# Optimization experiments

Hardware: AMD Instinct MI355X
Metric: run time of the kernel (lower is better)

The kernel has to match this reference:

```python
import jax, jax.numpy as jnp
import numpy as np
import math

B, S, E, H, D, L, HF = 8, 1024, 512, 8, 64, 6, 2048
EPS = 1e-5
INF = 1000000.0


def _gelu(x):
    # custom tanh-approx gelu from the source
    return 0.5 * x * (1 + jnp.tanh(math.sqrt(2 / math.pi) * (x + 0.044715 * x ** 3)))


def _layernorm(x, gamma, beta):
    mean = jnp.mean(x, axis=-1, keepdims=True)
    var = jnp.mean((x - mean) ** 2, axis=-1, keepdims=True)
    return gamma * ((x - mean) / jnp.sqrt(var + EPS)) + beta


def setup_inputs() -> dict:
    key = jax.random.key(0)
    ks = jax.random.split(key, 10)
    scale = 0.02
    x = jax.random.normal(ks[0], (B, S, E), dtype=jnp.float32)
    att_mask = jax.random.randint(ks[1], (B, S), 0, 2) == 1
    WQ = jax.random.normal(ks[2], (L, E, E), dtype=jnp.float32) * scale
    WK = jax.random.normal(ks[3], (L, E, E), dtype=jnp.float32) * scale
    WV = jax.random.normal(ks[4], (L, E, E), dtype=jnp.float32) * scale
    WO = jax.random.normal(ks[5], (L, E, E), dtype=jnp.float32) * scale
    W1 = jax.random.normal(ks[6], (L, HF, E), dtype=jnp.float32) * scale
    W2 = jax.random.normal(ks[7], (L, E, HF), dtype=jnp.float32) * scale
    bQ = jnp.zeros((L, E)); bK = jnp.zeros((L, E)); bV = jnp.zeros((L, E)); bO = jnp.zeros((L, E))
    b1 = jnp.zeros((L, HF)); b2 = jnp.zeros((L, E))
    g1 = jnp.ones((L, E)); bt1 = jnp.zeros((L, E))
    g2 = jnp.ones((L, E)); bt2 = jnp.zeros((L, E))
    return {"x": x, "att_mask": att_mask, "WQ": WQ, "bQ": bQ, "WK": WK, "bK": bK,
            "WV": WV, "bV": bV, "WO": WO, "bO": bO, "W1": W1, "b1": b1, "W2": W2,
            "b2": b2, "g1": g1, "bt1": bt1, "g2": g2, "bt2": bt2}


def reference(x, att_mask, WQ, bQ, WK, bK, WV, bV, WO, bO, W1, b1, W2, b2, g1, bt1, g2, bt2):
    # additive mask applied to scores: score - (~mask) * infinity, broadcast over (B,1,1,S)
    inv_att = (~att_mask).astype(x.dtype)[:, None, None, :] * INF
    inv_sqrt_d = 1.0 / math.sqrt(D)
    for l in range(L):
        # --- multi-head self-attention ---
        q = (jnp.einsum('bse,fe->bsf', x, WQ[l]) + bQ[l]).reshape(B, S, H, D).transpose(0, 2, 1, 3)
        k = (jnp.einsum('bse,fe->bsf', x, WK[l]) + bK[l]).reshape(B, S, H, D).transpose(0, 2, 1, 3)
        v = (jnp.einsum('bse,fe->bsf', x, WV[l]) + bV[l]).reshape(B, S, H, D).transpose(0, 2, 1, 3)
        score = jnp.einsum('bhsd,bhtd->bhst', q, k) * inv_sqrt_d - inv_att
        attn = jax.nn.softmax(score, axis=-1)
        o = jnp.einsum('bhst,bhtd->bhsd', attn, v).transpose(0, 2, 1, 3).reshape(B, S, E)
        o = jnp.einsum('bse,fe->bsf', o, WO[l]) + bO[l]
        x = _layernorm(x + o, g1[l], bt1[l])
        # --- pointwise feed-forward ---
        h = _gelu(jnp.einsum('bse,fe->bsf', x, W1[l]) + b1[l])
        f = jnp.einsum('bsf,ef->bse', h, W2[l]) + b2[l]
        x = _layernorm(x + f, g2[l], bt2[l])
    return x
```

## Files before the change

### kernel.cpp

```cpp
#include <hip/hip_runtime.h>
#include <cstdint>
#include <cstddef>

#define NB 8
#define NS 1024
#define NE 512
#define NH 8
#define ND 64
#define NL 6
#define NHF 2048
#define NROW (NB*NS)

typedef __bf16 bf16_t;
typedef __bf16 bf8v __attribute__((ext_vector_type(8)));
typedef __bf16 bf4v __attribute__((ext_vector_type(4)));
typedef float  f4   __attribute__((ext_vector_type(4)));

extern "C" __device__ float __ocml_native_exp2_f32(float);
#define EXP2F __ocml_native_exp2_f32
#define LOG2E 1.4426950408889634f

__device__ __forceinline__ void async_copy16(const bf16_t* g, bf16_t* l) {
    __builtin_amdgcn_global_load_lds(
        (const __attribute__((address_space(1))) void*)g,
        (__attribute__((address_space(3))) void*)l,
        16, 0, 0);
}

__device__ __forceinline__ float gelu_f(float x) {
    const float s = fmaf(0.044715f * x * x, x, x);
    const float e = EXP2F(-2.3022081995f * s);
    return x * __builtin_amdgcn_rcpf(1.0f + e);
}

template<int BN, int ACT, int OUT>
__device__ __forceinline__ void gemm_core(
    bf16_t* __restrict__ sm,
    const bf16_t* __restrict__ A, const bf16_t* __restrict__ Bm,
    const float* __restrict__ bias, bf16_t* __restrict__ Cb,
    int m0, int n0, int N, int K)
{
    constexpr int JN = BN / 32, WSPAN = BN / 2;
    bf16_t* As = sm;
    bf16_t* Bs = sm + 2*128*64;
    const int tid  = threadIdx.x;
    const int lane = tid & 63;
    const int wave = tid >> 6;
    const int wm = wave >> 1, wn = wave & 1;
    const int quad = lane >> 4, l16 = lane & 15;
    const int srow = tid >> 3;
    const int scol = (((tid & 7) ^ (srow & 7)) << 3);

    f4 acc[4][JN] = {};

    const bf16_t* Ag = A  + (size_t)(m0 + srow) * K + scol;
    const bf16_t* Bg = Bm + (size_t)(n0 + srow) * K + scol;
    const int sw = (l16 & 7);

    auto stage = [&](int buf, int kt) {
#pragma unroll
        for (int r = 0; r < 4; ++r)
            async_copy16(Ag + (size_t)r * 32 * K + kt, As + buf*8192 + tid*8 + r*2048);
#pragma unroll
        for (int r = 0; r < BN/32; ++r)
            async_copy16(Bg + (size_t)r * 32 * K + kt, Bs + buf*(BN*64) + tid*8 + r*2048);
    };

    stage(0, 0);
    int buf = 0;
    for (int kt = 0; kt < K; kt += 64, buf ^= 1) {
        __syncthreads();
        if (kt + 64 < K) stage(buf ^ 1, kt + 64);
        const bf16_t* Ab = As + buf*8192;
        const bf16_t* Bb = Bs + buf*(BN*64);
#pragma unroll
        for (int s = 0; s < 2; ++s) {
            const int c8 = ((s*4 + quad) ^ sw) * 8;
            bf8v af[4], bfv[JN];
#pragma unroll
            for (int i = 0; i < 4; ++i)
                af[i] = *(const bf8v*)(Ab + (wm*64 + i*16 + l16)*64 + c8);
#pragma unroll
            for (int j = 0; j < JN; ++j)
                bfv[j] = *(const bf8v*)(Bb + (wn*WSPAN + j*16 + l16)*64 + c8);
#pragma unroll
            for (int i = 0; i < 4; ++i)
#pragma unroll
                for (int j = 0; j < JN; ++j)
                    acc[i][j] = __builtin_amdgcn_mfma_f32_16x16x32_bf16(bfv[j], af[i], acc[i][j], 0, 0, 0);
        }
    }

#pragma unroll
    for (int i = 0; i < 4; ++i) {
        const int mi = m0 + wm*64 + i*16 + l16;
        const size_t m = (size_t)mi;
#pragma unroll
        for (int j = 0; j < JN; ++j) {
            const int nb = n0 + wn*WSPAN + j*16 + quad*4;
            const f4 bv = *(const f4*)(bias + nb);
            f4 v = acc[i][j] + bv;
            if (ACT) {
#pragma unroll
                for (int r = 0; r < 4; ++r) v[r] = gelu_f(v[r]);
            }
            bf4v* cp = (bf4v*)(Cb + m * (size_t)N + nb);
            bf4v o;
            if (OUT == 2) {
                const bf4v old = *cp;
#pragma unroll
                for (int r = 0; r < 4; ++r) o[r] = (bf16_t)((float)old[r] + v[r]);
            } else {
#pragma unroll
                for (int r = 0; r < 4; ++r) o[r] = (bf16_t)v[r];
            }
            *cp = o;
        }
    }
}

template<int BN, int ACT, int OUT>
__global__ __launch_bounds__(256)
void gemm_bt_k(const bf16_t* __restrict__ A, const bf16_t* __restrict__ Bm,
               const float* __restrict__ bias, bf16_t* __restrict__ Cb, int N, int K)
{
    __shared__ __align__(16) bf16_t smem[2*128*64 + 2*BN*64];
    gemm_core<BN, ACT, OUT>(smem, A, Bm, bias, Cb,
                            blockIdx.x * 128, blockIdx.y * BN, N, K);
}

__global__ __launch_bounds__(512, 2)
void gemm_rmw_ln_k(const bf16_t* __restrict__ A, const bf16_t* __restrict__ Bm,
                   const float* __restrict__ bias, bf16_t* __restrict__ xb,
                   const float* __restrict__ gamma, const float* __restrict__ beta,
                   float* __restrict__ fout, int wf, int K)
{
    __shared__ __align__(16) bf16_t As[2*32*64];
    __shared__ __align__(16) bf16_t Bs[2*512*64];
    __shared__ float wsum[8][32], wssq[8][32];
    const int tid  = threadIdx.x;
    const int lane = tid & 63;
    const int wave = tid >> 6;
    const int quad = lane >> 4, l16 = lane & 15;
    const int sw = l16 & 7;
    const int srow = tid >> 3;
    const int scol = ((tid & 7) ^ (srow & 7)) << 3;
    const int m0 = blockIdx.x * 32;

    const bf16_t* Ag = A  + (size_t)(m0 + srow) * K + scol;
    const bf16_t* Bg = Bm + (size_t)srow * K + scol;

    f4 acc[2][4] = {};

    auto stage = [&](int buf, int kt) {
        if (tid < 256)
            async_copy16(Ag + kt, As + buf*2048 + tid*8);
#pragma unroll
        for (int r = 0; r < 8; ++r)
            async_copy16(Bg + (size_t)r * 64 * K + kt, Bs + buf*32768 + (r*512 + tid)*8);
    };

    stage(0, 0);
    int buf = 0;
    for (int kt = 0; kt < K; kt += 64, buf ^= 1) {
        __syncthreads();
        if (kt + 64 < K) stage(buf ^ 1, kt + 64);
        const bf16_t* Ab = As + buf*2048;
        const bf16_t* Bb = Bs + buf*32768;
#pragma unroll
        for (int s = 0; s < 2; ++s) {
            const int c8 = ((s*4 + quad) ^ sw) * 8;
            bf8v af[2], bfv[4];
#pragma unroll
            for (int i = 0; i < 2; ++i)
                af[i] = *(const bf8v*)(Ab + (i*16 + l16)*64 + c8);
#pragma unroll
            for (int j = 0; j < 4; ++j)
                bfv[j] = *(const bf8v*)(Bb + (wave*64 + j*16 + l16)*64 + c8);
#pragma unroll
            for (int i = 0; i < 2; ++i)
#pragma unroll
                for (int j = 0; j < 4; ++j)
                    acc[i][j] = __builtin_amdgcn_mfma_f32_16x16x32_bf16(bfv[j], af[i], acc[i][j], 0, 0, 0);
        }
    }

    f4 v[2][4];
    float ps[2], pss[2];
#pragma unroll
    for (int i = 0; i < 2; ++i) {
        ps[i] = 0.f; pss[i] = 0.f;
        const size_t m = (size_t)(m0 + i*16 + l16);
#pragma unroll
        for (int j = 0; j < 4; ++j) {
            const int nb = wave*64 + j*16 + quad*4;
            const f4 bv = *(const f4*)(bias + nb);
            const bf4v old = *(const bf4v*)(xb + m * NE + nb);
            f4 t = acc[i][j] + bv;
#pragma unroll
            for (int r = 0; r < 4; ++r) {
                t[r] += (float)old[r];
                ps[i]  += t[r];
                pss[i] += t[r] * t[r];
            }
            v[i][j] = t;
        }
        ps[i]  += __shfl_xor(ps[i], 16, 64);
        ps[i]  += __shfl_xor(ps[i], 32, 64);
        pss[i] += __shfl_xor(pss[i], 16, 64);
        pss[i] += __shfl_xor(pss[i], 32, 64);
    }
    if (quad == 0) {
#pragma unroll
        for (int i = 0; i < 2; ++i) {
            wsum[wave][i*16 + l16] = ps[i];
            wssq[wave][i*16 + l16] = pss[i];
        }
    }
    __syncthreads();
#pragma unroll
    for (int i = 0; i < 2; ++i) {
        const int row = i*16 + l16;
        float s = 0.f, ss = 0.f;
#pragma unroll
        for (int w = 0; w < 8; ++w) { s += wsum[w][row]; ss += wssq[w][row]; }
        const float mean = s * (1.0f / NE);
        const float var  = ss * (1.0f / NE) - mean * mean;
        const float inv  = rsqrtf(var + 1e-5f);
        const size_t m = (size_t)(m0 + row);
#pragma unroll
        for (int j = 0; j < 4; ++j) {
            const int nb = wave*64 + j*16 + quad*4;
            const f4 gm = *(const f4*)(gamma + nb);
            const f4 bt = *(const f4*)(beta + nb);
            f4 o;
            bf4v ob;
#pragma unroll
            for (int r = 0; r < 4; ++r) {
                o[r]  = gm[r] * ((v[i][j][r] - mean) * inv) + bt[r];
                ob[r] = (bf16_t)o[r];
            }
            *(bf4v*)(xb + m * NE + nb) = ob;
            if (wf) *(f4*)(fout + m * NE + nb) = o;
        }
    }
}

__global__ __launch_bounds__(256, 2)
void gemm_qkv_k(const bf16_t* __restrict__ A,
                const bf16_t* __restrict__ wq, const bf16_t* __restrict__ wk, const bf16_t* __restrict__ wv,
                const float* __restrict__ bq, const float* __restrict__ bk, const float* __restrict__ bv,
                bf16_t* __restrict__ Q, bf16_t* __restrict__ K, bf16_t* __restrict__ Vt,
                const unsigned short* __restrict__ rank)
{
    __shared__ __align__(16) bf16_t As_[2*128*64];
    __shared__ __align__(16) bf16_t Bs_[3][2*64*64];
    const int tid  = threadIdx.x;
    const int lane = tid & 63;
    const int wave = tid >> 6;
    const int wm = wave >> 1, wn = wave & 1;
    const int quad = lane >> 4, l16 = lane & 15;
    const int sw = l16 & 7;
    const int srow = tid >> 3;
    const int scol = (((tid & 7) ^ (srow & 7)) << 3);
    const int m0 = blockIdx.x * 128, n0 = blockIdx.y * 64;

    const bf16_t* Ag = A + (size_t)(m0 + srow) * NE + scol;
    const bf16_t* Wg0 = wq + (size_t)(n0 + srow) * NE + scol;
    const bf16_t* Wg1 = wk + (size_t)(n0 + srow) * NE + scol;
    const bf16_t* Wg2 = wv + (size_t)(n0 + srow) * NE + scol;

    f4 acc[3][4][2] = {};

    auto stage = [&](int buf, int kt) {
#pragma unroll
        for (int r = 0; r < 4; ++r)
            async_copy16(Ag + (size_t)r*32*NE + kt, As_ + buf*8192 + tid*8 + r*2048);
#pragma unroll
        for (int r = 0; r < 2; ++r) {
            async_copy16(Wg0 + (size_t)r*32*NE + kt, Bs_[0] + buf*4096 + tid*8 + r*2048);
            async_copy16(Wg1 + (size_t)r*32*NE + kt, Bs_[1] + buf*4096 + tid*8 + r*2048);
            async_copy16(Wg2 + (size_t)r*32*NE + kt, Bs_[2] + buf*4096 + tid*8 + r*2048);
        }
    };

    stage(0, 0);
    int buf = 0;
    for (int kt = 0; kt < NE; kt += 64, buf ^= 1) {
        __syncthreads();
        if (kt + 64 < NE) stage(buf ^ 1, kt + 64);
        const bf16_t* Ab = As_ + buf*8192;
#pragma unroll
        for (int s = 0; s < 2; ++s) {
            const int c8 = ((s*4 + quad) ^ sw) * 8;
            bf8v af[4];
#pragma unroll
            for (int i = 0; i < 4; ++i)
                af[i] = *(const bf8v*)(Ab + (wm*64 + i*16 + l16)*64 + c8);
#pragma unroll
            for (int mat = 0; mat < 3; ++mat) {
                const bf16_t* Bb = Bs_[mat] + buf*4096;
                const bf8v b0 = *(const bf8v*)(Bb + (wn*32      + l16)*64 + c8);
                const bf8v b1 = *(const bf8v*)(Bb + (wn*32 + 16 + l16)*64 + c8);
                if (mat < 2) {
#pragma unroll
                    for (int i = 0; i < 4; ++i) {
                        acc[mat][i][0] = __builtin_amdgcn_mfma_f32_16x16x32_bf16(b0, af[i], acc[mat][i][0], 0, 0, 0);
                        acc[mat][i][1] = __builtin_amdgcn_mfma_f32_16x16x32_bf16(b1, af[i], acc[mat][i][1], 0, 0, 0);
                    }
                } else {
#pragma unroll
                    for (int i = 0; i < 4; ++i) {
                        acc[2][i][0] = __builtin_amdgcn_mfma_f32_16x16x32_bf16(af[i], b0, acc[2][i][0], 0, 0, 0);
                        acc[2][i][1] = __builtin_amdgcn_mfma_f32_16x16x32_bf16(af[i], b1, acc[2][i][1], 0, 0, 0);
                    }
                }
            }
        }
    }

#pragma unroll
    for (int i = 0; i < 4; ++i) {
        const int mi = m0 + wm*64 + i*16 + l16;
        const int mk = (mi & ~1023) + (int)rank[mi];
#pragma unroll
        for (int j = 0; j < 2; ++j) {
            const int nb = n0 + wn*32 + j*16 + quad*4;
            const f4 vq = acc[0][i][j] + *(const f4*)(bq + nb);
            const f4 vk = acc[1][i][j] + *(const f4*)(bk + nb);
            bf4v oq, ok;
#pragma unroll
            for (int r = 0; r < 4; ++r) { oq[r] = (bf16_t)vq[r]; ok[r] = (bf16_t)vk[r]; }
            *(bf4v*)(Q + (size_t)mi * NE + nb) = oq;
            *(bf4v*)(K + (size_t)mk * NE + nb) = ok;
        }
    }
#pragma unroll
    for (int j = 0; j < 2; ++j) {
        const int n = n0 + wn*32 + j*16 + l16;
        const float bvv = bv[n];
#pragma unroll
        for (int i = 0; i < 4; ++i) {
            const int mbase = m0 + wm*64 + i*16 + quad*4;
            const size_t b8h = (size_t)((mbase >> 10)*8 + (n >> 6));
            bf16_t* rowp = Vt + (b8h*64 + (size_t)(n & 63))*1024;
#pragma unroll
            for (int r = 0; r < 4; ++r)
                rowp[rank[mbase + r]] = (bf16_t)(acc[2][i][j][r] + bvv);
        }
    }
}

template<int ACT, int OUT>
__device__ __forceinline__ void gemm256_core(
    bf16_t* __restrict__ sm,
    const bf16_t* __restrict__ A, const bf16_t* __restrict__ Bm,
    const float* __restrict__ bias, bf16_t* __restrict__ Cb,
    int m0, int n0, int N, int K)
{
    const int tid  = threadIdx.x;
    const int lane = tid & 63;
    const int wave = tid >> 6;
    const int wm = wave >> 2, wn = wave & 3;
    const int quad = lane >> 4, l16 = lane & 15;
    const int sw = l16 & 7;
    const int srow = tid >> 3;
    const int scol = ((tid & 7) ^ (srow & 7)) << 3;

    bf16_t* As = sm;
    bf16_t* Bs = sm + 4 * 8192;

    const bf16_t* Ag = A  + (size_t)(m0 + srow) * K + scol;
    const bf16_t* Bg = Bm + (size_t)(n0 + srow) * K + scol;

    auto stageA = [&](int d, int h, int kt) {
        bf16_t* dst = As + (d*2 + h) * 8192 + tid * 8;
        const bf16_t* src = Ag + (size_t)(h * 128) * K + kt;
        async_copy16(src, dst);
        async_copy16(src + (size_t)64 * K, dst + 4096);
    };
    auto stageB = [&](int d, int h, int kt) {
        bf16_t* dst = Bs + (d*2 + h) * 8192 + tid * 8;
        const bf16_t* src = Bg + (size_t)(h * 128) * K + kt;
        async_copy16(src, dst);
        async_copy16(src + (size_t)64 * K, dst + 4096);
    };

    const int nt = K >> 6;

    f4 acc[8][4] = {};
    bf8v bfr[4][2], al[4][2], ah[4][2];

    auto mfmaQ = [&](const bf8v (&af)[4][2], int fb, int gb) {
#pragma unroll
        for (int kh = 0; kh < 2; ++kh)
#pragma unroll
            for (int f = 0; f < 4; ++f)
#pragma unroll
                for (int g = 0; g < 2; ++g)
                    acc[fb+f][gb+g] = __builtin_amdgcn_mfma_f32_16x16x32_bf16(bfr[gb+g][kh], af[f][kh], acc[fb+f][gb+g], 0, 0, 0);
    };

    stageB(0, 0, 0);  stageB(0, 1, 0);  stageA(0, 0, 0);  stageA(0, 1, 0);
    stageB(1, 0, 64); stageB(1, 1, 64); stageA(1, 0, 64);
    asm volatile("s_waitcnt vmcnt(6)" ::: "memory");
    __builtin_amdgcn_s_barrier();

    for (int t = 0; t < nt; ++t) {
        const int d = t & 1;
        const int kt2 = (t + 2) << 6;
        const bf16_t* Ab = As + (d*2 + wm) * 8192;
        const bf16_t* Bb = Bs + (d*2 + (wn >> 1)) * 8192 + (wn & 1) * 4096;

#pragma unroll
        for (int g = 0; g < 4; ++g)
#pragma unroll
            for (int kh = 0; kh < 2; ++kh)
                bfr[g][kh] = *(const bf8v*)(Bb + (g*16 + l16)*64 + (((kh*4 + quad) ^ sw) << 3));
#pragma unroll
        for (int f = 0; f < 4; ++f)
#pragma unroll
            for (int kh = 0; kh < 2; ++kh)
                al[f][kh] = *(const bf8v*)(Ab + (f*16 + l16)*64 + (((kh*4 + quad) ^ sw) << 3));
        if (t + 1 < nt) stageA(d ^ 1, 1, (t + 1) << 6);
        __builtin_amdgcn_s_barrier();
        __builtin_amdgcn_s_setprio(1);
        mfmaQ(al, 0, 0);
        __builtin_amdgcn_s_setprio(0);
        asm volatile("s_waitcnt lgkmcnt(0)" ::: "memory");
        __builtin_amdgcn_s_barrier();

#pragma unroll
        for (int f = 0; f < 4; ++f)
#pragma unroll
            for (int kh = 0; kh < 2; ++kh)
                ah[f][kh] = *(const bf8v*)(Ab + ((f + 4)*16 + l16)*64 + (((kh*4 + quad) ^ sw) << 3));
        if (t + 2 < nt) stageB(d, 0, kt2);
        __builtin_amdgcn_s_barrier();
        __builtin_amdgcn_s_setprio(1);
        mfmaQ(ah, 4, 0);
        __builtin_amdgcn_s_setprio(0);
        asm volatile("s_waitcnt lgkmcnt(0)" ::: "memory");
        __builtin_amdgcn_s_barrier();

        if (t + 2 < nt) stageB(d, 1, kt2);
        __builtin_amdgcn_s_barrier();
        __builtin_amdgcn_s_setprio(1);
        mfmaQ(al, 0, 2);
        __builtin_amdgcn_s_setprio(0);
        asm volatile("s_waitcnt lgkmcnt(0)" ::: "memory");
        __builtin_amdgcn_s_barrier();

        if (t + 2 < nt) stageA(d, 0, kt2);
        __builtin_amdgcn_s_barrier();
        __builtin_amdgcn_s_setprio(1);
        mfmaQ(ah, 4, 2);
        __builtin_amdgcn_s_setprio(0);
        asm volatile("s_waitcnt lgkmcnt(0)" ::: "memory");
        if (t + 1 < nt) {
            if (t + 2 < nt) asm volatile("s_waitcnt vmcnt(6)" ::: "memory");
            else            asm volatile("s_waitcnt vmcnt(0)" ::: "memory");
        }
        __builtin_amdgcn_s_barrier();
    }

#pragma unroll
    for (int f = 0; f < 8; ++f) {
        const int mi = m0 + wm*128 + f*16 + l16;
        const size_t m = (size_t)mi;
#pragma unroll
        for (int g = 0; g < 4; ++g) {
            const int nb = n0 + wn*64 + g*16 + quad*4;
            const f4 bv = *(const f4*)(bias + nb);
            f4 v = acc[f][g] + bv;
            if (ACT) {
#pragma unroll
                for (int r = 0; r < 4; ++r) v[r] = gelu_f(v[r]);
            }
            bf4v* cp = (bf4v*)(Cb + m * (size_t)N + nb);
            bf4v o;
            if (OUT == 2) {
                const bf4v old = *cp;
#pragma unroll
                for (int r = 0; r < 4; ++r) o[r] = (bf16_t)((float)old[r] + v[r]);
            } else {
#pragma unroll
                for (int r = 0; r < 4; ++r) o[r] = (bf16_t)v[r];
            }
            *cp = o;
        }
    }
}

template<int ACT, int OUT>
__global__ __launch_bounds__(512, 2)
void gemm256_k(const bf16_t* __restrict__ A, const bf16_t* __restrict__ Bm,
               const float* __restrict__ bias, bf16_t* __restrict__ Cb, int N, int K)
{
    __shared__ __align__(16) bf16_t smem[8 * 8192];
    gemm256_core<ACT, OUT>(smem, A, Bm, bias, Cb,
                           blockIdx.x * 256, blockIdx.y * 256, N, K);
}

__global__ __launch_bounds__(64)
void pack_k(const int* __restrict__ m, unsigned short* __restrict__ rank,
            int* __restrict__ cntpad, float* __restrict__ maskp)
{
    const int b = blockIdx.x, lane = threadIdx.x;
    unsigned long long bals[16];
    int cnt = 0;
#pragma unroll
    for (int c = 0; c < 16; ++c) {
        const bool mk = m[b*NS + c*64 + lane] != 0;
        bals[c] = __ballot(mk);
        cnt += __popcll(bals[c]);
    }
    int u = 0, kk = 0;
#pragma unroll
    for (int c = 0; c < 16; ++c) {
        const unsigned long long bal = bals[c];
        const bool mk = (bal >> lane) & 1;
        const int pu = __popcll(bal & ((1ull << lane) - 1));
        const int r = mk ? (u + pu) : (cnt + kk + (lane - pu));
        rank[b*NS + c*64 + lane] = (unsigned short)r;
        const int cb = __popcll(bal);
        u += cb; kk += 64 - cb;
    }
    if (lane == 0) {
        int cp = (cnt + 63) & ~63;
        cntpad[b] = cp < 64 ? 64 : cp;
    }
#pragma unroll
    for (int c = 0; c < 16; ++c) {
        const int j = c*64 + lane;
        maskp[b*NS + j] = (j < cnt) ? 0.0f : -1.0e6f * LOG2E;
    }
}

__global__ __launch_bounds__(256)
void attn_k(const bf16_t* __restrict__ Q, const bf16_t* __restrict__ Kg,
            const bf16_t* __restrict__ Vt, const float* __restrict__ maskf,
            const int* __restrict__ cntpad, bf16_t* __restrict__ O)
{
    __shared__ __align__(16) bf16_t Ks[2][64*64];
    __shared__ __align__(16) bf16_t Vs[2][64*64];
    __shared__ __align__(16) bf16_t Ps[4][32*64];
    const int tid  = threadIdx.x;
    const int lane = tid & 63;
    const int wave = tid >> 6;
    const int quad = lane >> 4, l16 = lane & 15;
    const int sw = l16 & 7;
    const int bh = blockIdx.x;
    const int b = bh >> 3, h = bh & 7;
    const int q0 = blockIdx.y * 128;
    const int kend = cntpad[b];

    bf8v qf[2][2];
#pragma unroll
    for (int qi = 0; qi < 2; ++qi) {
        const bf16_t* Qp = Q + (size_t)(b*NS + q0 + wave*32 + qi*16 + l16) * NE + h*ND;
        qf[qi][0] = *(const bf8v*)(Qp + quad*8);
        qf[qi][1] = *(const bf8v*)(Qp + 32 + quad*8);
    }

    f4 oacc[2][4] = {};
    float rs[2] = {0.f, 0.f};

    const int srow = tid >> 3;
    const int scol = (((tid & 7) ^ (srow & 7)) << 3);
    const float c1 = 0.125f * LOG2E;

    auto stage = [&](int buf, int kt) {
#pragma unroll
        for (int r = 0; r < 2; ++r) {
            async_copy16(Kg + (size_t)(b*NS + kt + r*32 + srow) * NE + h*ND + scol,
                         Ks[buf] + (r*256 + tid) * 8);
            async_copy16(Vt + (size_t)(bh*ND + r*32 + srow) * NS + kt + scol,
                         Vs[buf] + (r*256 + tid) * 8);
        }
    };

    stage(0, 0);
    int buf = 0;
    for (int kt = 0; kt < kend; kt += 64, buf ^= 1) {
        __syncthreads();
        if (kt + 64 < kend) stage(buf ^ 1, kt + 64);

        f4 sacc[2][4] = {};
        __builtin_amdgcn_s_setprio(1);
#pragma unroll
        for (int j = 0; j < 4; ++j) {
            bf8v kf0 = *(const bf8v*)(Ks[buf] + (j*16 + l16)*64 + ((quad    ) ^ sw)*8);
            bf8v kf1 = *(const bf8v*)(Ks[buf] + (j*16 + l16)*64 + ((quad + 4) ^ sw)*8);
#pragma unroll
            for (int qi = 0; qi < 2; ++qi) {
                sacc[qi][j] = __builtin_amdgcn_mfma_f32_16x16x32_bf16(kf0, qf[qi][0], sacc[qi][j], 0, 0, 0);
                sacc[qi][j] = __builtin_amdgcn_mfma_f32_16x16x32_bf16(kf1, qf[qi][1], sacc[qi][j], 0, 0, 0);
            }
        }
        __builtin_amdgcn_s_setprio(0);

        bf16_t* Pw = Ps[wave];
#pragma unroll
        for (int j = 0; j < 4; ++j) {
            const f4 mkv = *(const f4*)(maskf + b*NS + kt + j*16 + quad*4);
#pragma unroll
            for (int qi = 0; qi < 2; ++qi) {
                bf4v o;
#pragma unroll
                for (int r = 0; r < 4; ++r) {
                    const float p = EXP2F(fmaf(sacc[qi][j][r], c1, mkv[r]));
                    rs[qi] += p;
                    o[r] = (bf16_t)p;
                }
                const int row = qi*16 + l16;
                const int chunk = (j*2 + (quad >> 1)) ^ sw;
                *(bf4v*)(Pw + row*64 + chunk*8 + (quad & 1)*4) = o;
            }
        }

        __builtin_amdgcn_s_setprio(1);
#pragma unroll
        for (int ks = 0; ks < 2; ++ks) {
            bf8v pf[2];
#pragma unroll
            for (int qi = 0; qi < 2; ++qi)
                pf[qi] = *(const bf8v*)(Pw + (qi*16 + l16)*64 + ((ks*4 + quad) ^ sw)*8);
#pragma unroll
            for (int nt = 0; nt < 4; ++nt) {
                bf8v vf = *(const bf8v*)(Vs[buf] + (nt*16 + l16)*64 + ((ks*4 + quad) ^ sw)*8);
#pragma unroll
                for (int qi = 0; qi < 2; ++qi)
                    oacc[qi][nt] = __builtin_amdgcn_mfma_f32_16x16x32_bf16(vf, pf[qi], oacc[qi][nt], 0, 0, 0);
            }
        }
        __builtin_amdgcn_s_setprio(0);
    }

#pragma unroll
    for (int qi = 0; qi < 2; ++qi) {
        float s = rs[qi];
        s += __shfl_xor(s, 16, 64);
        s += __shfl_xor(s, 32, 64);
        const float inv = 1.0f / s;
        const size_t row = (size_t)(b*NS + q0 + wave*32 + qi*16 + l16);
#pragma unroll
        for (int nt = 0; nt < 4; ++nt) {
            bf4v o;
#pragma unroll
            for (int r = 0; r < 4; ++r) o[r] = (bf16_t)(oacc[qi][nt][r] * inv);
            *(bf4v*)(O + row * NE + h*ND + nt*16 + quad*4) = o;
        }
    }
}

__global__ __launch_bounds__(256)
void ln_k(bf16_t* __restrict__ xb,
          const float* __restrict__ gamma, const float* __restrict__ beta,
          float* __restrict__ fout, int wf)
{
    const int wave = threadIdx.x >> 6, lane = threadIdx.x & 63;
    const size_t row  = (size_t)blockIdx.x * 4 + wave;
    const size_t base = row * NE;
    const f4 g0 = *(const f4*)(gamma + lane*8);
    const f4 g1 = *(const f4*)(gamma + lane*8 + 4);
    const f4 b0 = *(const f4*)(beta  + lane*8);
    const f4 b1 = *(const f4*)(beta  + lane*8 + 4);
    const bf8v v = *(const bf8v*)(xb + base + lane*8);
    float xv[8], s = 0.f, ss = 0.f;
#pragma unroll
    for (int r = 0; r < 8; ++r) { xv[r] = (float)v[r]; s += xv[r]; ss += xv[r]*xv[r]; }
#pragma unroll
    for (int off = 32; off > 0; off >>= 1) {
        s  += __shfl_xor(s,  off, 64);
        ss += __shfl_xor(ss, off, 64);
    }
    const float mean = s * (1.0f / NE);
    const float var  = ss * (1.0f / NE) - mean * mean;
    const float inv  = rsqrtf(var + 1e-5f);
    f4 o0, o1;
    bf8v ob;
#pragma unroll
    for (int r = 0; r < 4; ++r) {
        o0[r] = g0[r] * ((xv[r]     - mean) * inv) + b0[r];
        o1[r] = g1[r] * ((xv[r + 4] - mean) * inv) + b1[r];
        ob[r]     = (bf16_t)o0[r];
        ob[r + 4] = (bf16_t)o1[r];
    }
    *(bf8v*)(xb + base + lane*8) = ob;
    if (wf) {
        *(f4*)(fout + base + lane*8)     = o0;
        *(f4*)(fout + base + lane*8 + 4) = o1;
    }
}

#define W4SZ ((size_t)NL*NE*NE/4)
#define WBSZ ((size_t)NL*NE*NHF/4)
#define XSZ  ((size_t)NROW*NE/4)
#define CVT_TOTAL (4*W4SZ + 2*WBSZ + XSZ)

__global__ void cvt_all(const float* __restrict__ wq, const float* __restrict__ wk,
                        const float* __restrict__ wv, const float* __restrict__ wo,
                        const float* __restrict__ w1, const float* __restrict__ w2,
                        const float* __restrict__ x,
                        bf16_t* __restrict__ owq, bf16_t* __restrict__ owk,
                        bf16_t* __restrict__ owv, bf16_t* __restrict__ owo,
                        bf16_t* __restrict__ ow1, bf16_t* __restrict__ ow2,
                        bf16_t* __restrict__ ox)
{
    size_t i = (size_t)blockIdx.x * 256 + threadIdx.x;
    if (i >= CVT_TOTAL) return;
    const float* src; bf16_t* dst;
    if      (i < 1*W4SZ)           { src = wq; dst = owq; }
    else if (i < 2*W4SZ)           { src = wk; dst = owk; i -= 1*W4SZ; }
    else if (i < 3*W4SZ)           { src = wv; dst = owv; i -= 2*W4SZ; }
    else if (i < 4*W4SZ)           { src = wo; dst = owo; i -= 3*W4SZ; }
    else if (i < 4*W4SZ + WBSZ)    { src = w1; dst = ow1; i -= 4*W4SZ; }
    else if (i < 4*W4SZ + 2*WBSZ)  { src = w2; dst = ow2; i -= 4*W4SZ + WBSZ; }
    else                           { src = x;  dst = ox;  i -= 4*W4SZ + 2*WBSZ; }
    const f4 v = ((const f4*)src)[i];
    bf4v o;
    o[0] = (bf16_t)v[0]; o[1] = (bf16_t)v[1]; o[2] = (bf16_t)v[2]; o[3] = (bf16_t)v[3];
    ((bf4v*)dst)[i] = o;
}

extern "C" void kernel_launch(void* const* d_in, const int* in_sizes, int n_in,
                              void* d_out, int out_size, void* d_ws, size_t ws_size,
                              hipStream_t stream)
{
    (void)in_sizes; (void)n_in; (void)out_size; (void)ws_size;
    const float* x   = (const float*)d_in[0];
    const int*   msk = (const int*)d_in[1];
    const float* WQ = (const float*)d_in[2];  const float* bQ  = (const float*)d_in[3];
    const float* WK = (const float*)d_in[4];  const float* bK  = (const float*)d_in[5];
    const float* WV = (const float*)d_in[6];  const float* bV  = (const float*)d_in[7];
    const float* WO = (const float*)d_in[8];  const float* bO  = (const float*)d_in[9];
    const float* W1 = (const float*)d_in[10]; const float* b1  = (const float*)d_in[11];
    const float* W2 = (const float*)d_in[12]; const float* b2  = (const float*)d_in[13];
    const float* g1 = (const float*)d_in[14]; const float* bt1 = (const float*)d_in[15];
    const float* g2 = (const float*)d_in[16]; const float* bt2 = (const float*)d_in[17];

    char* ws = (char*)d_ws;
    size_t off = 0;
    auto alloc = [&](size_t bytes) { char* p = ws + off; off += (bytes + 255) & ~(size_t)255; return p; };
    bf16_t* xb    = (bf16_t*)alloc((size_t)NROW*NE*2);
    bf16_t* Qb    = (bf16_t*)alloc((size_t)NROW*NE*2);
    bf16_t* Kb    = (bf16_t*)alloc((size_t)NROW*NE*2);
    bf16_t* Vtb   = (bf16_t*)alloc((size_t)NROW*NE*2);
    bf16_t* AOb   = (bf16_t*)alloc((size_t)NROW*NE*2);
    bf16_t* hb    = (bf16_t*)alloc((size_t)NROW*NHF*2);
    bf16_t* wqc   = (bf16_t*)alloc((size_t)NL*NE*NE*2);
    bf16_t* wkc   = (bf16_t*)alloc((size_t)NL*NE*NE*2);
    bf16_t* wvc   = (bf16_t*)alloc((size_t)NL*NE*NE*2);
    bf16_t* woc   = (bf16_t*)alloc((size_t)NL*NE*NE*2);
    bf16_t* w1c   = (bf16_t*)alloc((size_t)NL*NHF*NE*2);
    bf16_t* w2c   = (bf16_t*)alloc((size_t)NL*NE*NHF*2);
    float*  maskp = (float*) alloc((size_t)NB*NS*4);
    unsigned short* rankb = (unsigned short*)alloc((size_t)NB*NS*2);
    int*    cntp  = (int*)   alloc(NB*4);

    cvt_all<<<dim3((unsigned)((CVT_TOTAL + 255) / 256)), dim3(256), 0, stream>>>(
        WQ, WK, WV, WO, W1, W2, x, wqc, wkc, wvc, woc, w1c, w2c, xb);
    pack_k<<<dim3(NB), dim3(64), 0, stream>>>(msk, rankb, cntp, maskp);

    for (int l = 0; l < NL; ++l) {
        const bf16_t* wq  = wqc + (size_t)l*NE*NE;
        const bf16_t* wk  = wkc + (size_t)l*NE*NE;
        const bf16_t* wv  = wvc + (size_t)l*NE*NE;
        const bf16_t* wo  = woc + (size_t)l*NE*NE;
        const bf16_t* w1p = w1c + (size_t)l*NHF*NE;
        const bf16_t* w2p = w2c + (size_t)l*NE*NHF;
        const int last = (l == NL - 1);

        gemm_qkv_k<<<dim3(64, 8), dim3(256), 0, stream>>>(
            xb, wq, wk, wv, bQ + l*NE, bK + l*NE, bV + l*NE, Qb, Kb, Vtb, rankb);
        attn_k<<<dim3(64, 8), dim3(256), 0, stream>>>(Qb, Kb, Vtb, maskp, cntp, AOb);
        gemm_rmw_ln_k<<<dim3(256), dim3(512), 0, stream>>>(
            AOb, wo, bO + l*NE, xb, g1 + l*NE, bt1 + l*NE,
            nullptr, 0, NE);
        gemm256_k<1, 1><<<dim3(32, 8), dim3(512), 0, stream>>>(
            xb, w1p, b1 + l*NHF, hb, NHF, NE);
        gemm_bt_k<128, 0, 2><<<dim3(64, 4), dim3(256), 0, stream>>>(
            hb, w2p, b2 + l*NE, xb, NE, NHF);
        ln_k<<<dim3(NROW/4), dim3(256), 0, stream>>>(
            xb, g2 + l*NE, bt2 + l*NE, (float*)d_out, last);
    }
}
```

Before: 878.9 us.

## Remap block indices for XCD-aware L2 locality, fuse pack into convert, batch LN rows

Flattens the grids of the QKV GEMM, attention, FFN1 and FFN2 kernels to 1D and remaps block IDs so that consecutive tiles land on the same XCD (block id mod 8). The intent is better L2 reuse of shared A/B tiles and K/V panels. The mask pack kernel is folded into the conversion kernel to save one launch. The LayerNorm kernel now processes four rows per wave with a grid four times smaller. The remap relies on the hardware dispatching blocks round-robin across XCDs, and the grid sizes must stay divisible by 8.

```diff
diff --git a/kernel.cpp b/kernel.cpp
--- a/kernel.cpp
+++ b/kernel.cpp
@@ -122,11 +122,14 @@
 template<int BN, int ACT, int OUT>
 __global__ __launch_bounds__(256)
 void gemm_bt_k(const bf16_t* __restrict__ A, const bf16_t* __restrict__ Bm,
-               const float* __restrict__ bias, bf16_t* __restrict__ Cb, int N, int K)
+               const float* __restrict__ bias, bf16_t* __restrict__ Cb,
+               int N, int K, int nxb)
 {
     __shared__ __align__(16) bf16_t smem[2*128*64 + 2*BN*64];
+    const int d = blockIdx.x, q = gridDim.x >> 3;
+    const int L = (d & 7) * q + (d >> 3);
     gemm_core<BN, ACT, OUT>(smem, A, Bm, bias, Cb,
-                            blockIdx.x * 128, blockIdx.y * BN, N, K);
+                            (L % nxb) * 128, (L / nxb) * BN, N, K);
 }
 
 __global__ __launch_bounds__(512, 2)
@@ -263,7 +266,9 @@
     const int sw = l16 & 7;
     const int srow = tid >> 3;
     const int scol = (((tid & 7) ^ (srow & 7)) << 3);
-    const int m0 = blockIdx.x * 128, n0 = blockIdx.y * 64;
+    const int d = blockIdx.x;
+    const int L = (d & 7) * 64 + (d >> 3);
+    const int m0 = (L & 63) * 128, n0 = (L >> 6) * 64;
 
     const bf16_t* Ag = A + (size_t)(m0 + srow) * NE + scol;
     const bf16_t* Wg0 = wq + (size_t)(n0 + srow) * NE + scol;
@@ -498,43 +503,10 @@
                const float* __restrict__ bias, bf16_t* __restrict__ Cb, int N, int K)
 {
     __shared__ __align__(16) bf16_t smem[8 * 8192];
+    const int d = blockIdx.x;
+    const int L = (d & 7) * 32 + (d >> 3);
     gemm256_core<ACT, OUT>(smem, A, Bm, bias, Cb,
-                           blockIdx.x * 256, blockIdx.y * 256, N, K);
-}
-
-__global__ __launch_bounds__(64)
-void pack_k(const int* __restrict__ m, unsigned short* __restrict__ rank,
-            int* __restrict__ cntpad, float* __restrict__ maskp)
-{
-    const int b = blockIdx.x, lane = threadIdx.x;
-    unsigned long long bals[16];
-    int cnt = 0;
-#pragma unroll
-    for (int c = 0; c < 16; ++c) {
-        const bool mk = m[b*NS + c*64 + lane] != 0;
-        bals[c] = __ballot(mk);
-        cnt += __popcll(bals[c]);
-    }
-    int u = 0, kk = 0;
-#pragma unroll
-    for (int c = 0; c < 16; ++c) {
-        const unsigned long long bal = bals[c];
-        const bool mk = (bal >> lane) & 1;
-        const int pu = __popcll(bal & ((1ull << lane) - 1));
-        const int r = mk ? (u + pu) : (cnt + kk + (lane - pu));
-        rank[b*NS + c*64 + lane] = (unsigned short)r;
-        const int cb = __popcll(bal);
-        u += cb; kk += 64 - cb;
-    }
-    if (lane == 0) {
-        int cp = (cnt + 63) & ~63;
-        cntpad[b] = cp < 64 ? 64 : cp;
-    }
-#pragma unroll
-    for (int c = 0; c < 16; ++c) {
-        const int j = c*64 + lane;
-        maskp[b*NS + j] = (j < cnt) ? 0.0f : -1.0e6f * LOG2E;
-    }
+                           (L & 31) * 256, (L >> 5) * 256, N, K);
 }
 
 __global__ __launch_bounds__(256)
@@ -550,9 +522,11 @@
     const int wave = tid >> 6;
     const int quad = lane >> 4, l16 = lane & 15;
     const int sw = l16 & 7;
-    const int bh = blockIdx.x;
+    const int dd = blockIdx.x, tt = dd >> 3;
+    const int L = 8 * (dd & 7) + (tt & 7) + 64 * (tt >> 3);
+    const int bh = L & 63;
     const int b = bh >> 3, h = bh & 7;
-    const int q0 = blockIdx.y * 128;
+    const int q0 = (L >> 6) * 128;
     const int kend = cntpad[b];
 
     bf8v qf[2][2];
@@ -660,37 +634,40 @@
           float* __restrict__ fout, int wf)
 {
     const int wave = threadIdx.x >> 6, lane = threadIdx.x & 63;
-    const size_t row  = (size_t)blockIdx.x * 4 + wave;
-    const size_t base = row * NE;
     const f4 g0 = *(const f4*)(gamma + lane*8);
     const f4 g1 = *(const f4*)(gamma + lane*8 + 4);
     const f4 b0 = *(const f4*)(beta  + lane*8);
     const f4 b1 = *(const f4*)(beta  + lane*8 + 4);
-    const bf8v v = *(const bf8v*)(xb + base + lane*8);
-    float xv[8], s = 0.f, ss = 0.f;
-#pragma unroll
-    for (int r = 0; r < 8; ++r) { xv[r] = (float)v[r]; s += xv[r]; ss += xv[r]*xv[r]; }
-#pragma unroll
-    for (int off = 32; off > 0; off >>= 1) {
-        s  += __shfl_xor(s,  off, 64);
-        ss += __shfl_xor(ss, off, 64);
-    }
-    const float mean = s * (1.0f / NE);
-    const float var  = ss * (1.0f / NE) - mean * mean;
-    const float inv  = rsqrtf(var + 1e-5f);
-    f4 o0, o1;
-    bf8v ob;
-#pragma unroll
-    for (int r = 0; r < 4; ++r) {
-        o0[r] = g0[r] * ((xv[r]     - mean) * inv) + b0[r];
-        o1[r] = g1[r] * ((xv[r + 4] - mean) * inv) + b1[r];
-        ob[r]     = (bf16_t)o0[r];
-        ob[r + 4] = (bf16_t)o1[r];
-    }
-    *(bf8v*)(xb + base + lane*8) = ob;
-    if (wf) {
-        *(f4*)(fout + base + lane*8)     = o0;
-        *(f4*)(fout + base + lane*8 + 4) = o1;
+#pragma unroll
+    for (int rr = 0; rr < 4; ++rr) {
+        const size_t row  = (size_t)blockIdx.x * 16 + wave * 4 + rr;
+        const size_t base = row * NE;
+        const bf8v v = *(const bf8v*)(xb + base + lane*8);
+        float xv[8], s = 0.f, ss = 0.f;
+#pragma unroll
+        for (int r = 0; r < 8; ++r) { xv[r] = (float)v[r]; s += xv[r]; ss += xv[r]*xv[r]; }
+#pragma unroll
+        for (int off = 32; off > 0; off >>= 1) {
+            s  += __shfl_xor(s,  off, 64);
+            ss += __shfl_xor(ss, off, 64);
+        }
+        const float mean = s * (1.0f / NE);
+        const float var  = ss * (1.0f / NE) - mean * mean;
+        const float inv  = rsqrtf(var + 1e-5f);
+        f4 o0, o1;
+        bf8v ob;
+#pragma unroll
+        for (int r = 0; r < 4; ++r) {
+            o0[r] = g0[r] * ((xv[r]     - mean) * inv) + b0[r];
+            o1[r] = g1[r] * ((xv[r + 4] - mean) * inv) + b1[r];
+            ob[r]     = (bf16_t)o0[r];
+            ob[r + 4] = (bf16_t)o1[r];
+        }
+        *(bf8v*)(xb + base + lane*8) = ob;
+        if (wf) {
+            *(f4*)(fout + base + lane*8)     = o0;
+            *(f4*)(fout + base + lane*8 + 4) = o1;
+        }
     }
 }
 
@@ -698,16 +675,52 @@
 #define WBSZ ((size_t)NL*NE*NHF/4)
 #define XSZ  ((size_t)NROW*NE/4)
 #define CVT_TOTAL (4*W4SZ + 2*WBSZ + XSZ)
-
-__global__ void cvt_all(const float* __restrict__ wq, const float* __restrict__ wk,
-                        const float* __restrict__ wv, const float* __restrict__ wo,
-                        const float* __restrict__ w1, const float* __restrict__ w2,
-                        const float* __restrict__ x,
-                        bf16_t* __restrict__ owq, bf16_t* __restrict__ owk,
-                        bf16_t* __restrict__ owv, bf16_t* __restrict__ owo,
-                        bf16_t* __restrict__ ow1, bf16_t* __restrict__ ow2,
-                        bf16_t* __restrict__ ox)
-{
+#define CVT_BLOCKS ((unsigned)((CVT_TOTAL + 255) / 256))
+
+__global__ void cvt_pack_k(const float* __restrict__ wq, const float* __restrict__ wk,
+                           const float* __restrict__ wv, const float* __restrict__ wo,
+                           const float* __restrict__ w1, const float* __restrict__ w2,
+                           const float* __restrict__ x,
+                           bf16_t* __restrict__ owq, bf16_t* __restrict__ owk,
+                           bf16_t* __restrict__ owv, bf16_t* __restrict__ owo,
+                           bf16_t* __restrict__ ow1, bf16_t* __restrict__ ow2,
+                           bf16_t* __restrict__ ox,
+                           const int* __restrict__ m, unsigned short* __restrict__ rank,
+                           int* __restrict__ cntpad, float* __restrict__ maskp)
+{
+    if (blockIdx.x >= CVT_BLOCKS) {
+        if (threadIdx.x >= 64) return;
+        const int b = blockIdx.x - CVT_BLOCKS, lane = threadIdx.x;
+        unsigned long long bals[16];
+        int cnt = 0;
+#pragma unroll
+        for (int c = 0; c < 16; ++c) {
+            const bool mk = m[b*NS + c*64 + lane] != 0;
+            bals[c] = __ballot(mk);
+            cnt += __popcll(bals[c]);
+        }
+        int u = 0, kk = 0;
+#pragma unroll
+        for (int c = 0; c < 16; ++c) {
+            const unsigned long long bal = bals[c];
+            const bool mk = (bal >> lane) & 1;
+            const int pu = __popcll(bal & ((1ull << lane) - 1));
+            const int r = mk ? (u + pu) : (cnt + kk + (lane - pu));
+            rank[b*NS + c*64 + lane] = (unsigned short)r;
+            const int cb = __popcll(bal);
+            u += cb; kk += 64 - cb;
+        }
+        if (lane == 0) {
+            int cp = (cnt + 63) & ~63;
+            cntpad[b] = cp < 64 ? 64 : cp;
+        }
+#pragma unroll
+        for (int c = 0; c < 16; ++c) {
+            const int j = c*64 + lane;
+            maskp[b*NS + j] = (j < cnt) ? 0.0f : -1.0e6f * LOG2E;
+        }
+        return;
+    }
     size_t i = (size_t)blockIdx.x * 256 + threadIdx.x;
     if (i >= CVT_TOTAL) return;
     const float* src; bf16_t* dst;
@@ -759,9 +772,9 @@
     unsigned short* rankb = (unsigned short*)alloc((size_t)NB*NS*2);
     int*    cntp  = (int*)   alloc(NB*4);
 
-    cvt_all<<<dim3((unsigned)((CVT_TOTAL + 255) / 256)), dim3(256), 0, stream>>>(
-        WQ, WK, WV, WO, W1, W2, x, wqc, wkc, wvc, woc, w1c, w2c, xb);
-    pack_k<<<dim3(NB), dim3(64), 0, stream>>>(msk, rankb, cntp, maskp);
+    cvt_pack_k<<<dim3(CVT_BLOCKS + NB), dim3(256), 0, stream>>>(
+        WQ, WK, WV, WO, W1, W2, x, wqc, wkc, wvc, woc, w1c, w2c, xb,
+        msk, rankb, cntp, maskp);
 
     for (int l = 0; l < NL; ++l) {
         const bf16_t* wq  = wqc + (size_t)l*NE*NE;
@@ -772,17 +785,17 @@
         const bf16_t* w2p = w2c + (size_t)l*NE*NHF;
         const int last = (l == NL - 1);
 
-        gemm_qkv_k<<<dim3(64, 8), dim3(256), 0, stream>>>(
+        gemm_qkv_k<<<dim3(512), dim3(256), 0, stream>>>(
             xb, wq, wk, wv, bQ + l*NE, bK + l*NE, bV + l*NE, Qb, Kb, Vtb, rankb);
-        attn_k<<<dim3(64, 8), dim3(256), 0, stream>>>(Qb, Kb, Vtb, maskp, cntp, AOb);
+        attn_k<<<dim3(512), dim3(256), 0, stream>>>(Qb, Kb, Vtb, maskp, cntp, AOb);
         gemm_rmw_ln_k<<<dim3(256), dim3(512), 0, stream>>>(
             AOb, wo, bO + l*NE, xb, g1 + l*NE, bt1 + l*NE,
             nullptr, 0, NE);
-        gemm256_k<1, 1><<<dim3(32, 8), dim3(512), 0, stream>>>(
+        gemm256_k<1, 1><<<dim3(256), dim3(512), 0, stream>>>(
             xb, w1p, b1 + l*NHF, hb, NHF, NE);
-        gemm_bt_k<128, 0, 2><<<dim3(64, 4), dim3(256), 0, stream>>>(
-            hb, w2p, b2 + l*NE, xb, NE, NHF);
-        ln_k<<<dim3(NROW/4), dim3(256), 0, stream>>>(
+        gemm_bt_k<128, 0, 2><<<dim3(256), dim3(256), 0, stream>>>(
+            hb, w2p, b2 + l*NE, xb, NE, NHF, 64);
+        ln_k<<<dim3(NROW/16), dim3(256), 0, stream>>>(
             xb, g2 + l*NE, bt2 + l*NE, (float*)d_out, last);
     }
 }
```

Measured after the change: 953.8 us. 1.09x slower.
